# Performance work log

Measured on AMD Instinct MI355X. Metric: run time of the kernel, lower is better.

## Reference

```python
import jax, jax.numpy as jnp
import numpy as np

MAX_HOPS = 3


def setup_inputs() -> dict:
    key = jax.random.key(0)
    ks = jax.random.split(key, 6)
    B, M, S = 128, 200, 20
    V, D = 100000, 128
    NC, CL = 10000, 10
    stories = jax.random.randint(ks[0], (B, M, S), 0, V, dtype=jnp.int64)
    queries = jax.random.randint(ks[1], (B, S), 0, V, dtype=jnp.int64)
    candidates = jax.random.randint(ks[2], (NC, CL), 0, V, dtype=jnp.int64)
    # 0.05 scale keeps hop softmax logits in a sane range
    A_tab = jax.random.normal(ks[3], (V, D), dtype=jnp.float32) * 0.05
    W_tab = jax.random.normal(ks[4], (V, D), dtype=jnp.float32) * 0.05
    H_w = jax.random.normal(ks[5], (D, D), dtype=jnp.float32) * 0.05
    return {"stories": stories, "queries": queries, "candidates": candidates,
            "A_tab": A_tab, "W_tab": W_tab, "H_w": H_w}


def reference(stories, queries, candidates, A_tab, W_tab, H_w):
    # padding_idx=0: embedding row 0 is zero
    A = A_tab.at[0].set(0.0)
    W = W_tab.at[0].set(0.0)
    # query encoding: gather + sum-pool -> [B, D]
    u = jnp.sum(A[queries], axis=1)
    # memory encoding: [B, M, D] (same A table each hop, as in the source)
    m = jnp.sum(A[stories], axis=2)
    for _ in range(MAX_HOPS):
        dotted = jnp.einsum('bmd,bd->bm', m, u)          # attention logits
        probs = jax.nn.softmax(dotted, axis=1)           # [B, M]
        o = jnp.einsum('bm,bmd->bd', probs, m)           # weighted memory sum
        u = jnp.tanh(u @ H_w.T + o)                      # Linear(no bias) + tanh
    cand_sum = jnp.sum(W[candidates], axis=1)            # [NC, D]
    logits = u @ cand_sum.T                              # [B, NC]
    return logits
```

## Files before the change

kernel.cpp:

```cpp
#include <hip/hip_runtime.h>
#include <hip/hip_bf16.h>
#include <math.h>

#define BB 128
#define MM 200
#define SS 20
#define DD 128
#define NC 10000
#define CL 10
#define CTILE 40

__global__ void k_detect(const int* __restrict__ q, int* __restrict__ flag) {
    int lane = threadIdx.x;
    int zc = 0;
    for (int i = lane; i < 1024; i += 64) zc += (q[2 * i + 1] == 0);
    for (int off = 32; off; off >>= 1) zc += __shfl_down(zc, off);
    if (lane == 0) *flag = (zc >= 512) ? 1 : 0;
}

__device__ __forceinline__ unsigned pack_bf16(float a, float b) {
    unsigned ua = __float_as_uint(a), ub = __float_as_uint(b);
    ua += 0x7fff + ((ua >> 16) & 1);
    ub += 0x7fff + ((ub >> 16) & 1);
    return (ua >> 16) | (ub & 0xffff0000u);
}
__device__ __forceinline__ float bflo(unsigned v) { return __uint_as_float(v << 16); }
__device__ __forceinline__ float bfhi(unsigned v) { return __uint_as_float(v & 0xffff0000u); }

__global__ __launch_bounds__(512) void k_fused(const int* __restrict__ stories,
                                               const int* __restrict__ queries,
                                               const int* __restrict__ cands,
                                               const float* __restrict__ A,
                                               const float* __restrict__ W,
                                               const float* __restrict__ Hw,
                                               float* __restrict__ uT,
                                               float* __restrict__ cand_buf,
                                               const int* __restrict__ flag) {
    __shared__ unsigned m_s[MM][DD / 2];
    __shared__ float u_s[DD];
    __shared__ float p_s[MM];
    __shared__ float o_part[8][DD];
    __shared__ float red_s;

    int b = blockIdx.x;
    int tid = threadIdx.x;
    int shift = *flag;

    if (b < BB) {
        int g = tid >> 5, l = tid & 31;
        for (int r = 0; r < 13; ++r) {
            int mm = g + (r << 4);
            if (mm < MM) {
                int toks[SS];
#pragma unroll
                for (int s = 0; s < SS; ++s)
                    toks[s] = stories[((size_t)((b * MM + mm) * SS + s)) << shift];
                float4 acc = make_float4(0.f, 0.f, 0.f, 0.f);
#pragma unroll
                for (int s = 0; s < SS; ++s) {
                    float4 v = ((const float4*)(A + (size_t)toks[s] * DD))[l];
                    float msk = toks[s] ? 1.f : 0.f;
                    acc.x = fmaf(msk, v.x, acc.x);
                    acc.y = fmaf(msk, v.y, acc.y);
                    acc.z = fmaf(msk, v.z, acc.z);
                    acc.w = fmaf(msk, v.w, acc.w);
                }
                m_s[mm][2 * l] = pack_bf16(acc.x, acc.y);
                m_s[mm][2 * l + 1] = pack_bf16(acc.z, acc.w);
            }
        }
        if (tid < DD) {
            float acc = 0.f;
#pragma unroll
            for (int s = 0; s < SS; ++s) {
                int tok = queries[((size_t)(b * SS + s)) << shift];
                float v = A[(size_t)tok * DD + tid];
                acc += tok ? v : 0.f;
            }
            u_s[tid] = acc;
        }
        __syncthreads();

        for (int hop = 0; hop < 3; ++hop) {
            if (tid < MM) {
                const float2* u2 = (const float2*)u_s;
                float acc = 0.f;
#pragma unroll 8
                for (int li = 0; li < 64; ++li) {
                    int j = (tid + li) & 63;
                    unsigned pv = m_s[tid][j];
                    float2 uv = u2[j];
                    acc += bflo(pv) * uv.x + bfhi(pv) * uv.y;
                }
                p_s[tid] = acc;
            }
            __syncthreads();
            if (tid < 64) {
                float v0 = p_s[tid], v1 = p_s[tid + 64], v2 = p_s[tid + 128];
                float v3 = (tid < 8) ? p_s[tid + 192] : -1e30f;
                float mx = fmaxf(fmaxf(v0, v1), fmaxf(v2, v3));
                for (int off = 32; off; off >>= 1) mx = fmaxf(mx, __shfl_down(mx, off));
                mx = __shfl(mx, 0);
                float e0 = __expf(v0 - mx), e1 = __expf(v1 - mx), e2 = __expf(v2 - mx);
                float e3 = (tid < 8) ? __expf(v3 - mx) : 0.f;
                float sm = e0 + e1 + e2 + e3;
                for (int off = 32; off; off >>= 1) sm += __shfl_down(sm, off);
                p_s[tid] = e0;
                p_s[tid + 64] = e1;
                p_s[tid + 128] = e2;
                if (tid < 8) p_s[tid + 192] = e3;
                if (tid == 0) red_s = 1.f / __shfl(sm, 0);
            }
            __syncthreads();
            {
                int c = tid & 63, h = tid >> 6;
                int mm0 = h * 25;
                float ax = 0.f, ay = 0.f;
#pragma unroll 5
                for (int k = 0; k < 25; ++k) {
                    unsigned pv = m_s[mm0 + k][c];
                    float p = p_s[mm0 + k];
                    ax = fmaf(p, bflo(pv), ax);
                    ay = fmaf(p, bfhi(pv), ay);
                }
                o_part[h][2 * c] = ax;
                o_part[h][2 * c + 1] = ay;
            }
            __syncthreads();
            float u_new = 0.f;
            if (tid < DD) {
                float o = 0.f;
#pragma unroll
                for (int h = 0; h < 8; ++h) o += o_part[h][tid];
                float acc = o * red_s;
                const float4* hrow = (const float4*)(Hw + tid * DD);
                const float4* u4 = (const float4*)u_s;
#pragma unroll 8
                for (int j = 0; j < DD / 4; ++j) {
                    float4 hv = hrow[j];
                    float4 uv = u4[j];
                    acc += hv.x * uv.x + hv.y * uv.y + hv.z * uv.z + hv.w * uv.w;
                }
                u_new = tanhf(acc);
            }
            __syncthreads();
            if (tid < DD) u_s[tid] = u_new;
            __syncthreads();
        }
        if (tid < DD) uT[tid * BB + b] = u_s[tid];
    } else {
        int bb = b - BB;
        int g = tid >> 5, l = tid & 31;
        for (int pass = 0; pass < 5; ++pass) {
            int row = (pass << 11) + bb * 16 + g;
            if (row < NC) {
                int toks[CL];
#pragma unroll
                for (int s = 0; s < CL; ++s)
                    toks[s] = cands[((size_t)(row * CL + s)) << shift];
                float4 acc = make_float4(0.f, 0.f, 0.f, 0.f);
#pragma unroll
                for (int s = 0; s < CL; ++s) {
                    float4 v = ((const float4*)(W + (size_t)toks[s] * DD))[l];
                    float msk = toks[s] ? 1.f : 0.f;
                    acc.x = fmaf(msk, v.x, acc.x);
                    acc.y = fmaf(msk, v.y, acc.y);
                    acc.z = fmaf(msk, v.z, acc.z);
                    acc.w = fmaf(msk, v.w, acc.w);
                }
                ((float4*)(cand_buf + (size_t)row * DD))[l] = acc;
            }
        }
    }
}

__global__ __launch_bounds__(128) void k_logits(const float* __restrict__ uT,
                                                const float* __restrict__ cs,
                                                float* __restrict__ out) {
    __shared__ float c_s[CTILE][DD];
    int c0 = blockIdx.x * CTILE;
    int tid = threadIdx.x;
#pragma unroll
    for (int j = 0; j < CTILE; ++j) c_s[j][tid] = cs[(size_t)(c0 + j) * DD + tid];
    __syncthreads();
    float acc[CTILE];
#pragma unroll
    for (int j = 0; j < CTILE; ++j) acc[j] = 0.f;
#pragma unroll 4
    for (int k = 0; k < DD; ++k) {
        float ub = uT[k * BB + tid];
#pragma unroll
        for (int j = 0; j < CTILE; ++j) acc[j] += ub * c_s[j][k];
    }
    float4* op = (float4*)(out + (size_t)tid * NC + c0);
#pragma unroll
    for (int j = 0; j < CTILE / 4; ++j)
        op[j] = make_float4(acc[4 * j], acc[4 * j + 1], acc[4 * j + 2], acc[4 * j + 3]);
}

extern "C" void kernel_launch(void* const* d_in, const int* in_sizes, int n_in,
                              void* d_out, int out_size, void* d_ws, size_t ws_size,
                              hipStream_t stream) {
    const int* stories = (const int*)d_in[0];
    const int* queries = (const int*)d_in[1];
    const int* cands   = (const int*)d_in[2];
    const float* A  = (const float*)d_in[3];
    const float* W  = (const float*)d_in[4];
    const float* Hw = (const float*)d_in[5];
    float* out = (float*)d_out;

    float* ws = (float*)d_ws;
    float* cand_buf = ws;
    float* uT_buf = cand_buf + (size_t)NC * DD;
    int* flag = (int*)(uT_buf + BB * DD);

    k_detect<<<1, 64, 0, stream>>>(queries, flag);
    k_fused<<<256, 512, 0, stream>>>(stories, queries, cands, A, W, Hw,
                                     uT_buf, cand_buf, flag);
    k_logits<<<NC / CTILE, 128, 0, stream>>>(uT_buf, cand_buf, out);
}
```

Before: 197.5 us.

## Convert A table to bf16, widen candidate grid, register-tile logits GEMM

Adds a pass that converts the whole A embedding table to bf16 (zeroing the padding row) so the story and query gathers move half as many bytes per row. Candidate-sum work now runs on 625 separate blocks instead of 128 looping blocks, and the detect kernel is folded into an inline check on 8 query samples. The logits kernel is rewritten as a 4x8 register-tiled outer product with a transposed shared tile. The conversion reads and writes the full 51 MB table on every call, which may cost more than the gather traffic it saves, and the sums lose some precision from bf16 inputs.

```diff
diff --git a/kernel.cpp b/kernel.cpp
--- a/kernel.cpp
+++ b/kernel.cpp
@@ -8,15 +8,7 @@
 #define DD 128
 #define NC 10000
 #define CL 10
-#define CTILE 40
-
-__global__ void k_detect(const int* __restrict__ q, int* __restrict__ flag) {
-    int lane = threadIdx.x;
-    int zc = 0;
-    for (int i = lane; i < 1024; i += 64) zc += (q[2 * i + 1] == 0);
-    for (int off = 32; off; off >>= 1) zc += __shfl_down(zc, off);
-    if (lane == 0) *flag = (zc >= 512) ? 1 : 0;
-}
+#define LCT 64
 
 __device__ __forceinline__ unsigned pack_bf16(float a, float b) {
     unsigned ua = __float_as_uint(a), ub = __float_as_uint(b);
@@ -27,57 +19,86 @@
 __device__ __forceinline__ float bflo(unsigned v) { return __uint_as_float(v << 16); }
 __device__ __forceinline__ float bfhi(unsigned v) { return __uint_as_float(v & 0xffff0000u); }
 
-__global__ __launch_bounds__(512) void k_fused(const int* __restrict__ stories,
-                                               const int* __restrict__ queries,
-                                               const int* __restrict__ cands,
-                                               const float* __restrict__ A,
-                                               const float* __restrict__ W,
-                                               const float* __restrict__ Hw,
-                                               float* __restrict__ uT,
-                                               float* __restrict__ cand_buf,
-                                               const int* __restrict__ flag) {
+__device__ __forceinline__ int detect_shift(const int* __restrict__ q) {
+    int zc = 0;
+#pragma unroll
+    for (int i = 0; i < 8; ++i) zc += (q[2 * i + 1] == 0);
+    return (zc >= 6) ? 1 : 0;
+}
+
+__global__ __launch_bounds__(512) void k_conv(const float* __restrict__ A,
+                                              unsigned* __restrict__ Abf) {
+    size_t t = (size_t)blockIdx.x * 512 + threadIdx.x;
+    const float4* in = (const float4*)(A + t * 8);
+    float4 a = in[0], b = in[1];
+    if (t * 8 < DD) {
+        a = make_float4(0.f, 0.f, 0.f, 0.f);
+        b = make_float4(0.f, 0.f, 0.f, 0.f);
+    }
+    uint4 o;
+    o.x = pack_bf16(a.x, a.y);
+    o.y = pack_bf16(a.z, a.w);
+    o.z = pack_bf16(b.x, b.y);
+    o.w = pack_bf16(b.z, b.w);
+    ((uint4*)(Abf + t * 4))[0] = o;
+}
+
+__global__ __launch_bounds__(512) void k_main(const int* __restrict__ stories,
+                                              const int* __restrict__ queries,
+                                              const int* __restrict__ cands,
+                                              const unsigned* __restrict__ Abf,
+                                              const float* __restrict__ W,
+                                              const float* __restrict__ Hw,
+                                              float* __restrict__ uT,
+                                              float* __restrict__ cand_buf) {
     __shared__ unsigned m_s[MM][DD / 2];
     __shared__ float u_s[DD];
     __shared__ float p_s[MM];
     __shared__ float o_part[8][DD];
     __shared__ float red_s;
 
-    int b = blockIdx.x;
+    int bid = blockIdx.x;
     int tid = threadIdx.x;
-    int shift = *flag;
-
-    if (b < BB) {
-        int g = tid >> 5, l = tid & 31;
-        for (int r = 0; r < 13; ++r) {
-            int mm = g + (r << 4);
+    int shift = detect_shift(queries);
+
+    if (bid < BB) {
+        int b = bid;
+        int g = tid >> 4, l = tid & 15;
+#pragma unroll
+        for (int r = 0; r < 7; ++r) {
+            int mm = g + (r << 5);
             if (mm < MM) {
                 int toks[SS];
 #pragma unroll
                 for (int s = 0; s < SS; ++s)
                     toks[s] = stories[((size_t)((b * MM + mm) * SS + s)) << shift];
-                float4 acc = make_float4(0.f, 0.f, 0.f, 0.f);
+                float a[8] = {0.f, 0.f, 0.f, 0.f, 0.f, 0.f, 0.f, 0.f};
 #pragma unroll
                 for (int s = 0; s < SS; ++s) {
-                    float4 v = ((const float4*)(A + (size_t)toks[s] * DD))[l];
-                    float msk = toks[s] ? 1.f : 0.f;
-                    acc.x = fmaf(msk, v.x, acc.x);
-                    acc.y = fmaf(msk, v.y, acc.y);
-                    acc.z = fmaf(msk, v.z, acc.z);
-                    acc.w = fmaf(msk, v.w, acc.w);
-                }
-                m_s[mm][2 * l] = pack_bf16(acc.x, acc.y);
-                m_s[mm][2 * l + 1] = pack_bf16(acc.z, acc.w);
+                    uint4 v = ((const uint4*)(Abf + (size_t)toks[s] * (DD / 2)))[l];
+                    a[0] += bflo(v.x); a[1] += bfhi(v.x);
+                    a[2] += bflo(v.y); a[3] += bfhi(v.y);
+                    a[4] += bflo(v.z); a[5] += bfhi(v.z);
+                    a[6] += bflo(v.w); a[7] += bfhi(v.w);
+                }
+                uint4 o;
+                o.x = pack_bf16(a[0], a[1]);
+                o.y = pack_bf16(a[2], a[3]);
+                o.z = pack_bf16(a[4], a[5]);
+                o.w = pack_bf16(a[6], a[7]);
+                *(uint4*)&m_s[mm][4 * l] = o;
             }
         }
         if (tid < DD) {
+            int d = tid;
             float acc = 0.f;
 #pragma unroll
             for (int s = 0; s < SS; ++s) {
                 int tok = queries[((size_t)(b * SS + s)) << shift];
-                float v = A[(size_t)tok * DD + tid];
-                acc += tok ? v : 0.f;
-            }
-            u_s[tid] = acc;
+                unsigned pv = Abf[(size_t)tok * (DD / 2) + (d >> 1)];
+                acc += (d & 1) ? bfhi(pv) : bflo(pv);
+            }
+            u_s[d] = acc;
         }
         __syncthreads();
 
@@ -147,55 +168,78 @@
             if (tid < DD) u_s[tid] = u_new;
             __syncthreads();
         }
-        if (tid < DD) uT[tid * BB + b] = u_s[tid];
+        if (tid < DD) uT[tid * BB + bid] = u_s[tid];
     } else {
-        int bb = b - BB;
         int g = tid >> 5, l = tid & 31;
-        for (int pass = 0; pass < 5; ++pass) {
-            int row = (pass << 11) + bb * 16 + g;
-            if (row < NC) {
-                int toks[CL];
-#pragma unroll
-                for (int s = 0; s < CL; ++s)
-                    toks[s] = cands[((size_t)(row * CL + s)) << shift];
-                float4 acc = make_float4(0.f, 0.f, 0.f, 0.f);
-#pragma unroll
-                for (int s = 0; s < CL; ++s) {
-                    float4 v = ((const float4*)(W + (size_t)toks[s] * DD))[l];
-                    float msk = toks[s] ? 1.f : 0.f;
-                    acc.x = fmaf(msk, v.x, acc.x);
-                    acc.y = fmaf(msk, v.y, acc.y);
-                    acc.z = fmaf(msk, v.z, acc.z);
-                    acc.w = fmaf(msk, v.w, acc.w);
-                }
-                ((float4*)(cand_buf + (size_t)row * DD))[l] = acc;
-            }
-        }
-    }
-}
-
-__global__ __launch_bounds__(128) void k_logits(const float* __restrict__ uT,
+        int row = (bid - BB) * 16 + g;
+        int toks[CL];
+#pragma unroll
+        for (int s = 0; s < CL; ++s)
+            toks[s] = cands[((size_t)(row * CL + s)) << shift];
+        float4 acc = make_float4(0.f, 0.f, 0.f, 0.f);
+#pragma unroll
+        for (int s = 0; s < CL; ++s) {
+            float4 v = ((const float4*)(W + (size_t)toks[s] * DD))[l];
+            float msk = toks[s] ? 1.f : 0.f;
+            acc.x = fmaf(msk, v.x, acc.x);
+            acc.y = fmaf(msk, v.y, acc.y);
+            acc.z = fmaf(msk, v.z, acc.z);
+            acc.w = fmaf(msk, v.w, acc.w);
+        }
+        ((float4*)(cand_buf + (size_t)row * DD))[l] = acc;
+    }
+}
+
+__global__ __launch_bounds__(256) void k_logits(const float* __restrict__ uT,
                                                 const float* __restrict__ cs,
                                                 float* __restrict__ out) {
-    __shared__ float c_s[CTILE][DD];
-    int c0 = blockIdx.x * CTILE;
+    __shared__ float c_s[DD][LCT + 4];
+    int c0 = blockIdx.x * LCT;
     int tid = threadIdx.x;
-#pragma unroll
-    for (int j = 0; j < CTILE; ++j) c_s[j][tid] = cs[(size_t)(c0 + j) * DD + tid];
+    {
+        int c = tid >> 2, l = tid & 3;
+        int row = c0 + c;
+        if (row >= NC) row = NC - 1;
+        const float4* rp = (const float4*)(cs + (size_t)row * DD);
+#pragma unroll
+        for (int i = 0; i < 8; ++i) {
+            int k = (l << 5) + (i << 2);
+            float4 v = rp[(l << 3) + i];
+            c_s[k][c] = v.x;
+            c_s[k + 1][c] = v.y;
+            c_s[k + 2][c] = v.z;
+            c_s[k + 3][c] = v.w;
+        }
+    }
     __syncthreads();
-    float acc[CTILE];
-#pragma unroll
-    for (int j = 0; j < CTILE; ++j) acc[j] = 0.f;
+    int tx = tid & 31, ty = tid >> 5;
+    const float* cb = &c_s[0][ty << 3];
+    const float4* up = (const float4*)(uT + (tx << 2));
+    float acc[4][8];
+#pragma unroll
+    for (int i = 0; i < 4; ++i)
+#pragma unroll
+        for (int j = 0; j < 8; ++j) acc[i][j] = 0.f;
 #pragma unroll 4
     for (int k = 0; k < DD; ++k) {
-        float ub = uT[k * BB + tid];
-#pragma unroll
-        for (int j = 0; j < CTILE; ++j) acc[j] += ub * c_s[j][k];
-    }
-    float4* op = (float4*)(out + (size_t)tid * NC + c0);
-#pragma unroll
-    for (int j = 0; j < CTILE / 4; ++j)
-        op[j] = make_float4(acc[4 * j], acc[4 * j + 1], acc[4 * j + 2], acc[4 * j + 3]);
+        float4 uv = up[k * (BB / 4)];
+        float4 ca = *(const float4*)(cb + k * (LCT + 4));
+        float4 cc = *(const float4*)(cb + k * (LCT + 4) + 4);
+        float uu[4] = {uv.x, uv.y, uv.z, uv.w};
+        float cv[8] = {ca.x, ca.y, ca.z, ca.w, cc.x, cc.y, cc.z, cc.w};
+#pragma unroll
+        for (int i = 0; i < 4; ++i)
+#pragma unroll
+            for (int j = 0; j < 8; ++j) acc[i][j] = fmaf(uu[i], cv[j], acc[i][j]);
+    }
+    if (c0 + (ty << 3) < NC) {
+#pragma unroll
+        for (int i = 0; i < 4; ++i) {
+            float* orow = out + (size_t)((tx << 2) + i) * NC + c0 + (ty << 3);
+            ((float4*)orow)[0] = make_float4(acc[i][0], acc[i][1], acc[i][2], acc[i][3]);
+            ((float4*)orow)[1] = make_float4(acc[i][4], acc[i][5], acc[i][6], acc[i][7]);
+        }
+    }
 }
 
 extern "C" void kernel_launch(void* const* d_in, const int* in_sizes, int n_in,
@@ -209,13 +253,12 @@
     const float* Hw = (const float*)d_in[5];
     float* out = (float*)d_out;
 
-    float* ws = (float*)d_ws;
-    float* cand_buf = ws;
+    unsigned* Abf = (unsigned*)d_ws;
+    float* cand_buf = (float*)(Abf + 100000 * (DD / 2));
     float* uT_buf = cand_buf + (size_t)NC * DD;
-    int* flag = (int*)(uT_buf + BB * DD);
-
-    k_detect<<<1, 64, 0, stream>>>(queries, flag);
-    k_fused<<<256, 512, 0, stream>>>(stories, queries, cands, A, W, Hw,
-                                     uT_buf, cand_buf, flag);
-    k_logits<<<NC / CTILE, 128, 0, stream>>>(uT_buf, cand_buf, out);
-}
+
+    k_conv<<<100000 * DD / 8 / 512, 512, 0, stream>>>(A, Abf);
+    k_main<<<BB + NC / 16, 512, 0, stream>>>(stories, queries, cands, Abf, W, Hw,
+                                             uT_buf, cand_buf);
+    k_logits<<<(NC + LCT - 1) / LCT, 256, 0, stream>>>(uT_buf, cand_buf, out);
+}
```

Result: faster. 184.6 us (-6.5%).
